# Kernel optimization log

Measured on AMD Instinct MI355X. Metric: run time of the kernel, lower is better.

## Reference

```python
import jax, jax.numpy as jnp
import numpy as np

T, B, M, H, NH = 4, 8, 1024, 768, 12
HD = H // NH
KMAX = 10


def _ln(x, s, b):
    mu = x.mean(-1, keepdims=True)
    var = ((x - mu) ** 2).mean(-1, keepdims=True)
    return (x - mu) * jax.lax.rsqrt(var + 1e-5) * s + b


def setup_inputs() -> dict:
    key = jax.random.key(0)
    ks = jax.random.split(key, 10)
    init = lambda k, shp: jax.random.normal(k, shp, jnp.float32) * 0.02
    return {
        'x': jax.random.normal(ks[0], (B, M, H), jnp.float32),
        'overlap': jax.random.randint(ks[1], (B, M, M), 0, KMAX + 1, jnp.int32),
        'lp': -jax.random.uniform(ks[2], (B, M), jnp.float32) * 10.0,
        'ln1_s': jnp.ones((T, H)), 'ln1_b': jnp.zeros((T, H)),
        'Wqkv': init(ks[3], (T, H, 3 * H)),
        'Wout': init(ks[4], (T, H, H)), 'bout': jnp.zeros((T, H)),
        'ln2_s': jnp.ones((T, H)), 'ln2_b': jnp.zeros((T, H)),
        'W1': init(ks[5], (T, H, 4 * H)), 'b1': jnp.zeros((T, 4 * H)),
        'W2': init(ks[6], (T, 4 * H, H)), 'b2': jnp.zeros((T, H)),
        'lno_s': jnp.ones((H,)), 'lno_b': jnp.zeros((H,)),
        'ov_emb': init(ks[7], (KMAX + 1,)),
        'ht_alpha': jnp.ones((1,), jnp.float32),
    }


def reference(x, overlap, lp, ln1_s, ln1_b, Wqkv, Wout, bout, ln2_s, ln2_b,
              W1, b1, W2, b2, lno_s, lno_b, ov_emb, ht_alpha):
    lp_c = jnp.clip(lp, -30.0, 0.0)                      # [B,M]
    ov = ov_emb[jnp.minimum(overlap, KMAX)]              # [B,M,M]
    bias = (ov - ht_alpha[0] * lp_c[:, None, :])[:, None]  # [B,1,M,M]
    scale = 1.0 / jnp.sqrt(jnp.float32(HD))
    for t in range(T):
        r = _ln(x, ln1_s[t], ln1_b[t])
        q, k, v = jnp.split(r @ Wqkv[t], 3, axis=-1)
        q = q.reshape(B, M, NH, HD).transpose(0, 2, 1, 3)
        k = k.reshape(B, M, NH, HD).transpose(0, 2, 1, 3)
        v = v.reshape(B, M, NH, HD).transpose(0, 2, 1, 3)
        s = jnp.einsum('bhqd,bhkd->bhqk', q, k) * scale + bias
        a = jax.nn.softmax(s, axis=-1)
        o = jnp.einsum('bhqk,bhkd->bhqd', a, v).transpose(0, 2, 1, 3).reshape(B, M, H)
        x = x + o @ Wout[t] + bout[t]
        h = _ln(x, ln2_s[t], ln2_b[t])
        x = x + jax.nn.gelu(h @ W1[t] + b1[t], approximate=False) @ W2[t] + b2[t]
    x = _ln(x, lno_s, lno_b)
    w = jax.nn.softmax(-lp_c, axis=1)                    # HT weights over m tokens
    return jnp.einsum('bm,bmh->bh', w, x)
```

## Files before the change

### kernel.cpp

```cpp
#include <hip/hip_runtime.h>
#include <hip/hip_bf16.h>
#include <math.h>

#define TT 4
#define BB 8
#define MM 1024
#define HH 768
#define NHEAD 12
#define HDIM 64
#define NTOK 8192
#define H3 2304
#define H4 3072

typedef __attribute__((ext_vector_type(8))) short bf16x8;
typedef __attribute__((ext_vector_type(4))) float f32x4;
typedef __attribute__((ext_vector_type(4))) unsigned short u16x4;

#define GLOBAL_AS(p) ((const __attribute__((address_space(1))) void*)(p))
#define LDS_AS(p)    ((__attribute__((address_space(3))) void*)(p))

__device__ __forceinline__ unsigned short f2bf(float f) {
  union { float f; unsigned u; } v; v.f = f;
  unsigned r = v.u + 0x7fffu + ((v.u >> 16) & 1u);
  return (unsigned short)(r >> 16);
}

__device__ __forceinline__ unsigned cvt_pk_bf16(float lo, float hi) {
  unsigned r;
  asm("v_cvt_pk_bf16_f32 %0, %1, %2" : "=v"(r) : "v"(lo), "v"(hi));
  return r;
}

__device__ __forceinline__ float fast_exp2(float x) {
#if __has_builtin(__builtin_amdgcn_exp2f)
  return __builtin_amdgcn_exp2f(x);
#else
  return exp2f(x);
#endif
}

__device__ __forceinline__ f32x4 mfma16(bf16x8 a, bf16x8 b, f32x4 c) {
  return __builtin_amdgcn_mfma_f32_16x16x32_bf16(a, b, c, 0, 0, 0);
}

__device__ __forceinline__ float block_sum256(float v, float* sh) {
  #pragma unroll
  for (int off = 32; off > 0; off >>= 1) v += __shfl_down(v, off);
  if ((threadIdx.x & 63) == 0) sh[threadIdx.x >> 6] = v;
  __syncthreads();
  v = sh[0] + sh[1] + sh[2] + sh[3];
  __syncthreads();
  return v;
}

__device__ __forceinline__ float block_max256(float v, float* sh) {
  #pragma unroll
  for (int off = 32; off > 0; off >>= 1) v = fmaxf(v, __shfl_down(v, off));
  if ((threadIdx.x & 63) == 0) sh[threadIdx.x >> 6] = v;
  __syncthreads();
  v = fmaxf(fmaxf(sh[0], sh[1]), fmaxf(sh[2], sh[3]));
  __syncthreads();
  return v;
}

__global__ __launch_bounds__(256) void wconv_kernel(const float* __restrict__ W,
                                                    unsigned short* __restrict__ Wt,
                                                    int K, int N) {
  __shared__ float tile[32][33];
  const int n0 = blockIdx.x * 32, k0 = blockIdx.y * 32;
  const int tx = threadIdx.x, ty = threadIdx.y;
  #pragma unroll
  for (int j = 0; j < 4; j++)
    tile[ty + j*8][tx] = W[(size_t)(k0 + ty + j*8) * N + n0 + tx];
  __syncthreads();
  #pragma unroll
  for (int j = 0; j < 4; j++)
    Wt[(size_t)(n0 + ty + j*8) * K + k0 + tx] = f2bf(tile[tx][ty + j*8]);
}

__global__ __launch_bounds__(256) void ln_kernel(const float* __restrict__ x,
                                                 const float* __restrict__ s,
                                                 const float* __restrict__ b,
                                                 unsigned short* __restrict__ out) {
  __shared__ float sh[4];
  const int row = blockIdx.x;
  const int tid = threadIdx.x;
  const float* xr = x + (size_t)row * HH;
  float v[3];
  float sum = 0.f;
  #pragma unroll
  for (int j = 0; j < 3; j++) { v[j] = xr[tid + j*256]; sum += v[j]; }
  sum = block_sum256(sum, sh);
  const float mu = sum * (1.f/768.f);
  float ss = 0.f;
  #pragma unroll
  for (int j = 0; j < 3; j++) { float d = v[j] - mu; ss += d*d; }
  ss = block_sum256(ss, sh);
  const float rstd = rsqrtf(ss * (1.f/768.f) + 1e-5f);
  #pragma unroll
  for (int j = 0; j < 3; j++) {
    int col = tid + j*256;
    out[(size_t)row * HH + col] = f2bf((v[j]-mu)*rstd*s[col] + b[col]);
  }
}

template<int EPI>
__global__ __launch_bounds__(256) void gemm_kernel(const unsigned short* __restrict__ A,
                                                   const unsigned short* __restrict__ Bt,
                                                   unsigned short* __restrict__ outB,
                                                   float* __restrict__ outF,
                                                   const float* __restrict__ bias,
                                                   int Ng, int Kg, int nx) {
  __shared__ unsigned short a_lds[2][128*64];
  __shared__ unsigned short b_lds[2][128*64];
  const int tid = threadIdx.x;
  const int w = tid >> 6, l = tid & 63;
  const int nwg = gridDim.x;
  const int lin = blockIdx.x;
  const int L = (lin & 7) * (nwg >> 3) + (lin >> 3);
  const int m0 = (L / nx) * 128, n0 = (L % nx) * 128;

  const int wr = (w >> 1) * 64, wc = (w & 1) * 64;
  const int l15 = l & 15, lhi = l >> 4;
  const int srow = w*32 + (l >> 3);
  const int schunk = (l & 7) ^ (l >> 3);
  const int scol = schunk << 3;

  f32x4 acc[4][4] = {};
  const int nk = Kg >> 6;
  int cur = 0;

  #pragma unroll
  for (int i = 0; i < 4; i++) {
    const unsigned short* gsa = A  + (size_t)(m0 + srow + i*8)*Kg + scol;
    const unsigned short* gsb = Bt + (size_t)(n0 + srow + i*8)*Kg + scol;
    __builtin_amdgcn_global_load_lds(GLOBAL_AS(gsa), LDS_AS(&a_lds[0][w*2048 + i*512]), 16, 0, 0);
    __builtin_amdgcn_global_load_lds(GLOBAL_AS(gsb), LDS_AS(&b_lds[0][w*2048 + i*512]), 16, 0, 0);
  }
  __syncthreads();

  for (int t = 0; t < nk; t++) {
    if (t + 1 < nk) {
      const int ks = (t + 1) << 6;
      #pragma unroll
      for (int i = 0; i < 4; i++) {
        const unsigned short* gsa = A  + (size_t)(m0 + srow + i*8)*Kg + ks + scol;
        const unsigned short* gsb = Bt + (size_t)(n0 + srow + i*8)*Kg + ks + scol;
        __builtin_amdgcn_global_load_lds(GLOBAL_AS(gsa), LDS_AS(&a_lds[cur^1][w*2048 + i*512]), 16, 0, 0);
        __builtin_amdgcn_global_load_lds(GLOBAL_AS(gsb), LDS_AS(&b_lds[cur^1][w*2048 + i*512]), 16, 0, 0);
      }
    }
    const unsigned short* ab = &a_lds[cur][0];
    const unsigned short* bb = &b_lds[cur][0];
    #pragma unroll
    for (int kb = 0; kb < 2; kb++) {
      bf16x8 af[4], bfr[4];
      const int rc = (kb*4 + lhi) ^ (l15 & 7);
      #pragma unroll
      for (int rb = 0; rb < 4; rb++)
        af[rb] = *(const bf16x8*)&ab[(wr + rb*16 + l15)*64 + (rc << 3)];
      #pragma unroll
      for (int nb = 0; nb < 4; nb++)
        bfr[nb] = *(const bf16x8*)&bb[(wc + nb*16 + l15)*64 + (rc << 3)];
      #pragma unroll
      for (int rb = 0; rb < 4; rb++)
        #pragma unroll
        for (int nb = 0; nb < 4; nb++)
          acc[rb][nb] = mfma16(af[rb], bfr[nb], acc[rb][nb]);
    }
    __syncthreads();
    cur ^= 1;
  }

  const int lr = lhi << 2;
  #pragma unroll
  for (int rb = 0; rb < 4; rb++)
    #pragma unroll
    for (int nb = 0; nb < 4; nb++) {
      const int row = m0 + wr + rb*16 + lr;
      const int col = n0 + wc + nb*16 + l15;
      #pragma unroll
      for (int r = 0; r < 4; r++) {
        float v = acc[rb][nb][r];
        const size_t off = (size_t)(row + r)*Ng + col;
        if (EPI == 0) {
          outB[off] = f2bf(v);
        } else if (EPI == 1) {
          v += bias[col];
          float u = 0.79788456080287f * v * (1.f + 0.044715f * v * v);
          u = fminf(u, 15.f);
          float e = fast_exp2(u * 2.88539008177793f);
          float th = 1.f - 2.f / (e + 1.f);
          v = 0.5f * v * (1.f + th);
          outB[off] = f2bf(v);
        } else {
          v += bias[col] + outF[off];
          outF[off] = v;
        }
      }
    }
}

__global__ __launch_bounds__(256) void biasprep_kernel(const int* __restrict__ overlap,
                                                       const float* __restrict__ lp,
                                                       const float* __restrict__ ov_emb,
                                                       const float* __restrict__ ht_alpha,
                                                       float* __restrict__ biasP) {
  __shared__ float oe[11];
  if (threadIdx.x < 11) oe[threadIdx.x] = ov_emb[threadIdx.x] * 1.44269504088896f;
  __syncthreads();
  const float aL = ht_alpha[0] * 1.44269504088896f;
  const size_t base = ((size_t)blockIdx.x * 256 + threadIdx.x) * 4;
  const int b = (int)(base >> 20);
  const int k0 = (int)(base & 1023);
  int4 ov = *(const int4*)&overlap[base];
  float4 lv = *(const float4*)&lp[b * MM + k0];
  float4 o4;
  {
    int t0 = ov.x < 10 ? ov.x : 10; float c0 = fminf(fmaxf(lv.x, -30.f), 0.f); o4.x = oe[t0] - aL*c0;
    int t1 = ov.y < 10 ? ov.y : 10; float c1 = fminf(fmaxf(lv.y, -30.f), 0.f); o4.y = oe[t1] - aL*c1;
    int t2 = ov.z < 10 ? ov.z : 10; float c2 = fminf(fmaxf(lv.z, -30.f), 0.f); o4.z = oe[t2] - aL*c2;
    int t3 = ov.w < 10 ? ov.w : 10; float c3 = fminf(fmaxf(lv.w, -30.f), 0.f); o4.w = oe[t3] - aL*c3;
  }
  *(float4*)&biasP[base] = o4;
}

__global__ __launch_bounds__(256) void attn_kernel(const unsigned short* __restrict__ qkv,
                                                   const float* __restrict__ biasP,
                                                   unsigned short* __restrict__ obuf) {
  __shared__ unsigned short k_lds[2][64*64];
  __shared__ unsigned short v_lds[2][64*64];
  __shared__ unsigned short pmat[4][32*64];

  const int tid = threadIdx.x;
  const int w = tid >> 6, l = tid & 63;
  const int lin = blockIdx.x;
  const int L = (lin & 7) * 96 + (lin >> 3);
  const int h = L % 12;
  const int qb = (L / 12) & 7;
  const int b = L / 96;
  const int q0w = qb*128 + w*32;
  const int l15 = l & 15, lhi = l >> 4;
  const float SC = 0.125f * 1.44269504088896f;

  const int kr_s = l >> 3;
  const int schunk = (l & 7) ^ kr_s;
  const int dc = (l & 7) << 3;

  bf16x8 qf[2][2];
  #pragma unroll
  for (int rb = 0; rb < 2; rb++)
    #pragma unroll
    for (int kb = 0; kb < 2; kb++)
      qf[rb][kb] = *(const bf16x8*)&qkv[(size_t)(b*MM + q0w + rb*16 + l15)*H3 + h*HDIM + kb*32 + lhi*8];

  const float* brow[2];
  #pragma unroll
  for (int rb = 0; rb < 2; rb++)
    brow[rb] = biasP + (size_t)(b*MM + q0w + rb*16 + l15) * MM;

  f32x4 oacc[4][2] = {};
  float mrow[2] = {-INFINITY, -INFINITY};
  float lrow[2] = {0.f, 0.f};

  bf16x8 vcur[2];
  {
    #pragma unroll
    for (int i = 0; i < 2; i++) {
      const unsigned short* g = qkv + (size_t)(b*MM + i*32 + w*8 + kr_s)*H3 + h*HDIM + HH + schunk*8;
      __builtin_amdgcn_global_load_lds(GLOBAL_AS(g), LDS_AS(&k_lds[0][(i*32 + w*8)*64]), 16, 0, 0);
    }
    bf16x8 vr[2];
    #pragma unroll
    for (int i = 0; i < 2; i++)
      vr[i] = *(const bf16x8*)&qkv[(size_t)(b*MM + i*32 + w*8 + kr_s)*H3 + h*HDIM + 2*HH + dc];
    #pragma unroll
    for (int i = 0; i < 2; i++) {
      int kr = i*32 + w*8 + kr_s;
      #pragma unroll
      for (int j = 0; j < 8; j++) {
        int key = ((((dc >> 3) & 7) ^ j) & 7) << 3;
        v_lds[0][(dc + j)*64 + (kr ^ key)] = (unsigned short)(short)vr[i][j];
      }
    }
    #pragma unroll
    for (int i = 0; i < 2; i++)
      vcur[i] = *(const bf16x8*)&qkv[(size_t)(b*MM + 64 + i*32 + w*8 + kr_s)*H3 + h*HDIM + 2*HH + dc];
    __syncthreads();
  }

  for (int kt = 0; kt < 16; kt++) {
    const int cur = kt & 1;
    const int kbase = kt * 64;

    if (kt < 15) {
      #pragma unroll
      for (int i = 0; i < 2; i++) {
        int kr = i*32 + w*8 + kr_s;
        #pragma unroll
        for (int j = 0; j < 8; j++) {
          int key = ((((dc >> 3) & 7) ^ j) & 7) << 3;
          v_lds[cur^1][(dc + j)*64 + (kr ^ key)] = (unsigned short)(short)vcur[i][j];
        }
      }
      const int nbase = kbase + 64;
      #pragma unroll
      for (int i = 0; i < 2; i++) {
        const unsigned short* g = qkv + (size_t)(b*MM + nbase + i*32 + w*8 + kr_s)*H3 + h*HDIM + HH + schunk*8;
        __builtin_amdgcn_global_load_lds(GLOBAL_AS(g), LDS_AS(&k_lds[cur^1][(i*32 + w*8)*64]), 16, 0, 0);
      }
    }
    if (kt < 14) {
      const int n2 = kbase + 128;
      #pragma unroll
      for (int i = 0; i < 2; i++)
        vcur[i] = *(const bf16x8*)&qkv[(size_t)(b*MM + n2 + i*32 + w*8 + kr_s)*H3 + h*HDIM + 2*HH + dc];
    }
    f32x4 bregs[4][2];
    #pragma unroll
    for (int nb = 0; nb < 4; nb++)
      #pragma unroll
      for (int rb = 0; rb < 2; rb++)
        bregs[nb][rb] = *(const f32x4*)&brow[rb][kbase + nb*16 + lhi*4];

    f32x4 sacc[4][2] = {};
    const unsigned short* kb_lds = &k_lds[cur][0];
    __builtin_amdgcn_s_setprio(1);
    #pragma unroll
    for (int kb = 0; kb < 2; kb++) {
      bf16x8 ak[4];
      #pragma unroll
      for (int nb = 0; nb < 4; nb++) {
        int n = nb*16 + l15;
        ak[nb] = *(const bf16x8*)&kb_lds[n*64 + ((kb*32 + lhi*8) ^ ((n & 7) << 3))];
      }
      #pragma unroll
      for (int nb = 0; nb < 4; nb++)
        #pragma unroll
        for (int rb = 0; rb < 2; rb++)
          sacc[nb][rb] = mfma16(ak[nb], qf[rb][kb], sacc[nb][rb]);
    }
    __builtin_amdgcn_s_setprio(0);

    #pragma unroll
    for (int nb = 0; nb < 4; nb++)
      #pragma unroll
      for (int rb = 0; rb < 2; rb++)
        #pragma unroll
        for (int r = 0; r < 4; r++)
          sacc[nb][rb][r] = fmaf(sacc[nb][rb][r], SC, bregs[nb][rb][r]);

    float corrf[2];
    int defer[2];
    #pragma unroll
    for (int rb = 0; rb < 2; rb++) {
      float pm = sacc[0][rb][0];
      #pragma unroll
      for (int nb = 0; nb < 4; nb++)
        #pragma unroll
        for (int r = 0; r < 4; r++)
          pm = fmaxf(pm, sacc[nb][rb][r]);
      pm = fmaxf(pm, __shfl_xor(pm, 16));
      pm = fmaxf(pm, __shfl_xor(pm, 32));
      defer[rb] = __all(pm - mrow[rb] <= 8.0f);
      const float mnew = defer[rb] ? mrow[rb] : fmaxf(mrow[rb], pm);
      const float corr = defer[rb] ? 1.0f : fast_exp2(mrow[rb] - mnew);
      float rs = 0.f;
      #pragma unroll
      for (int nb = 0; nb < 4; nb++)
        #pragma unroll
        for (int r = 0; r < 4; r++) {
          float p = fast_exp2(sacc[nb][rb][r] - mnew);
          sacc[nb][rb][r] = p;
          rs += p;
        }
      rs += __shfl_xor(rs, 16);
      rs += __shfl_xor(rs, 32);
      mrow[rb] = mnew;
      lrow[rb] = lrow[rb]*corr + rs;
      corrf[rb] = corr;
    }
    #pragma unroll
    for (int rb = 0; rb < 2; rb++)
      if (!defer[rb]) {
        #pragma unroll
        for (int db = 0; db < 4; db++)
          #pragma unroll
          for (int r = 0; r < 4; r++)
            oacc[db][rb][r] *= corrf[rb];
      }

    unsigned short* pw = &pmat[w][0];
    #pragma unroll
    for (int nb = 0; nb < 4; nb++)
      #pragma unroll
      for (int rb = 0; rb < 2; rb++) {
        uint2 pk;
        pk.x = cvt_pk_bf16(sacc[nb][rb][0], sacc[nb][rb][1]);
        pk.y = cvt_pk_bf16(sacc[nb][rb][2], sacc[nb][rb][3]);
        *(uint2*)&pw[(rb*16 + l15)*64 + ((nb*16 + lhi*4) ^ ((l15 & 7) << 3))] = pk;
      }

    const unsigned short* vb_lds = &v_lds[cur][0];
    __builtin_amdgcn_s_setprio(1);
    #pragma unroll
    for (int kb = 0; kb < 2; kb++) {
      bf16x8 pb[2];
      #pragma unroll
      for (int rb = 0; rb < 2; rb++)
        pb[rb] = *(const bf16x8*)&pw[(rb*16 + l15)*64 + ((kb*32 + lhi*8) ^ ((l15 & 7) << 3))];
      bf16x8 av[4];
      #pragma unroll
      for (int db = 0; db < 4; db++) {
        int d = db*16 + l15;
        int key = ((((d >> 3) & 7) ^ (d & 7)) & 7) << 3;
        av[db] = *(const bf16x8*)&vb_lds[d*64 + ((kb*32 + lhi*8) ^ key)];
      }
      #pragma unroll
      for (int db = 0; db < 4; db++)
        #pragma unroll
        for (int rb = 0; rb < 2; rb++)
          oacc[db][rb] = mfma16(av[db], pb[rb], oacc[db][rb]);
    }
    __builtin_amdgcn_s_setprio(0);

    __syncthreads();
  }

  float inv[2] = { 1.f / lrow[0], 1.f / lrow[1] };
  unsigned short* pw = &pmat[w][0];
  #pragma unroll
  for (int db = 0; db < 4; db++)
    #pragma unroll
    for (int rb = 0; rb < 2; rb++) {
      uint2 pk;
      pk.x = cvt_pk_bf16(oacc[db][rb][0] * inv[rb], oacc[db][rb][1] * inv[rb]);
      pk.y = cvt_pk_bf16(oacc[db][rb][2] * inv[rb], oacc[db][rb][3] * inv[rb]);
      *(uint2*)&pw[(rb*16 + l15)*64 + ((db*16 + lhi*4) ^ ((l15 & 7) << 3))] = pk;
    }
  #pragma unroll
  for (int rep = 0; rep < 4; rep++) {
    int qq = rep*8 + (l >> 3);
    int d0 = (l & 7) << 3;
    bf16x8 vv = *(const bf16x8*)&pw[qq*64 + (d0 ^ ((qq & 7) << 3))];
    *(bf16x8*)&obuf[(size_t)(b*MM + q0w + qq)*HH + h*HDIM + d0] = vv;
  }
}

__global__ __launch_bounds__(256) void htw_kernel(const float* __restrict__ lp,
                                                  float* __restrict__ w_ht) {
  __shared__ float sh[4];
  const int b = blockIdx.x, tid = threadIdx.x;
  float vals[4];
  float mx = -INFINITY;
  #pragma unroll
  for (int j = 0; j < 4; j++) {
    float lv = lp[b*MM + tid + j*256];
    float lc = fminf(fmaxf(lv, -30.f), 0.f);
    vals[j] = -lc;
    mx = fmaxf(mx, vals[j]);
  }
  mx = block_max256(mx, sh);
  float se = 0.f;
  #pragma unroll
  for (int j = 0; j < 4; j++) { vals[j] = expf(vals[j] - mx); se += vals[j]; }
  se = block_sum256(se, sh);
  const float inv = 1.f / se;
  #pragma unroll
  for (int j = 0; j < 4; j++) w_ht[b*MM + tid + j*256] = vals[j] * inv;
}

__global__ __launch_bounds__(256) void final_partial_kernel(const float* __restrict__ xbuf,
                                                            const float* __restrict__ lno_s,
                                                            const float* __restrict__ lno_b,
                                                            const float* __restrict__ w_ht,
                                                            float* __restrict__ part) {
  __shared__ float sh[4];
  const int b = blockIdx.x >> 4;
  const int chunk = blockIdx.x & 15;
  const int tid = threadIdx.x;
  float acc[3] = {0.f, 0.f, 0.f};
  float sc[3], bc[3];
  #pragma unroll
  for (int j = 0; j < 3; j++) { sc[j] = lno_s[tid + j*256]; bc[j] = lno_b[tid + j*256]; }
  for (int rr = 0; rr < 64; rr++) {
    const int tok = b*MM + chunk*64 + rr;
    const float* xr = xbuf + (size_t)tok * HH;
    float v[3]; float sum = 0.f;
    #pragma unroll
    for (int j = 0; j < 3; j++) { v[j] = xr[tid + j*256]; sum += v[j]; }
    sum = block_sum256(sum, sh);
    const float mu = sum * (1.f/768.f);
    float ss = 0.f;
    #pragma unroll
    for (int j = 0; j < 3; j++) { float d = v[j] - mu; ss += d*d; }
    ss = block_sum256(ss, sh);
    const float rstd = rsqrtf(ss * (1.f/768.f) + 1e-5f);
    const float wgt = w_ht[b*MM + chunk*64 + rr];
    #pragma unroll
    for (int j = 0; j < 3; j++) acc[j] += wgt * ((v[j]-mu)*rstd*sc[j] + bc[j]);
  }
  #pragma unroll
  for (int j = 0; j < 3; j++) part[(size_t)blockIdx.x * HH + tid + j*256] = acc[j];
}

__global__ __launch_bounds__(256) void final_reduce_kernel(const float* __restrict__ part,
                                                           float* __restrict__ out) {
  const int b = blockIdx.x;
  const int col = blockIdx.y*256 + threadIdx.x;
  float s = 0.f;
  #pragma unroll
  for (int c = 0; c < 16; c++) s += part[(size_t)(b*16 + c) * HH + col];
  out[b*HH + col] = s;
}

extern "C" void kernel_launch(void* const* d_in, const int* in_sizes, int n_in,
                              void* d_out, int out_size, void* d_ws, size_t ws_size,
                              hipStream_t stream) {
  (void)in_sizes; (void)n_in;
  const float* x      = (const float*)d_in[0];
  const int*   overlap= (const int*)d_in[1];
  const float* lp     = (const float*)d_in[2];
  const float* ln1_s  = (const float*)d_in[3];
  const float* ln1_b  = (const float*)d_in[4];
  const float* Wqkv   = (const float*)d_in[5];
  const float* Wout   = (const float*)d_in[6];
  const float* bout   = (const float*)d_in[7];
  const float* ln2_s  = (const float*)d_in[8];
  const float* ln2_b  = (const float*)d_in[9];
  const float* W1     = (const float*)d_in[10];
  const float* b1     = (const float*)d_in[11];
  const float* W2     = (const float*)d_in[12];
  const float* b2     = (const float*)d_in[13];
  const float* lno_s  = (const float*)d_in[14];
  const float* lno_b  = (const float*)d_in[15];
  const float* ov_emb = (const float*)d_in[16];
  const float* ht_alpha = (const float*)d_in[17];
  float* out = (float*)d_out;

  char* ws = (char*)d_ws;
  float*          xbuf  = (float*)(ws + 0);
  unsigned short* lnout = (unsigned short*)(ws + 25165824);
  unsigned short* qkv   = (unsigned short*)(ws + 37748736);
  unsigned short* obuf  = (unsigned short*)(ws + 75497472);
  unsigned short* gbuf  = (unsigned short*)(ws + 88080384);
  unsigned short* wbuf  = (unsigned short*)(ws + 138412032);
  float*          w_ht  = (float*)(ws + 143130624);
  float*          part  = (float*)(ws + 143163392);
  const int prep_once = (ws_size >= (size_t)143556608 + (size_t)33554432);
  float*          biasP = prep_once ? (float*)(ws + 143556608) : (float*)gbuf;

  hipMemcpyAsync(xbuf, x, (size_t)NTOK * HH * sizeof(float), hipMemcpyDeviceToDevice, stream);
  htw_kernel<<<BB, 256, 0, stream>>>(lp, w_ht);
  if (prep_once)
    biasprep_kernel<<<(BB*MM*MM/4)/256, 256, 0, stream>>>(overlap, lp, ov_emb, ht_alpha, biasP);

  for (int t = 0; t < TT; t++) {
    wconv_kernel<<<dim3(H3/32, HH/32), dim3(32, 8), 0, stream>>>(Wqkv + (size_t)t*HH*H3, wbuf, HH, H3);
    ln_kernel<<<NTOK, 256, 0, stream>>>(xbuf, ln1_s + t*HH, ln1_b + t*HH, lnout);
    gemm_kernel<0><<<(H3/128)*(NTOK/128), 256, 0, stream>>>(lnout, wbuf, qkv, nullptr, nullptr, H3, HH, H3/128);
    if (!prep_once)
      biasprep_kernel<<<(BB*MM*MM/4)/256, 256, 0, stream>>>(overlap, lp, ov_emb, ht_alpha, biasP);
    attn_kernel<<<BB*NHEAD*(MM/128), 256, 0, stream>>>(qkv, biasP, obuf);
    wconv_kernel<<<dim3(HH/32, HH/32), dim3(32, 8), 0, stream>>>(Wout + (size_t)t*HH*HH, wbuf, HH, HH);
    gemm_kernel<2><<<(HH/128)*(NTOK/128), 256, 0, stream>>>(obuf, wbuf, nullptr, xbuf, bout + t*HH, HH, HH, HH/128);
    ln_kernel<<<NTOK, 256, 0, stream>>>(xbuf, ln2_s + t*HH, ln2_b + t*HH, lnout);
    wconv_kernel<<<dim3(H4/32, HH/32), dim3(32, 8), 0, stream>>>(W1 + (size_t)t*HH*H4, wbuf, HH, H4);
    gemm_kernel<1><<<(H4/128)*(NTOK/128), 256, 0, stream>>>(lnout, wbuf, gbuf, nullptr, b1 + t*H4, H4, HH, H4/128);
    wconv_kernel<<<dim3(HH/32, H4/32), dim3(32, 8), 0, stream>>>(W2 + (size_t)t*H4*HH, wbuf, H4, HH);
    gemm_kernel<2><<<(HH/128)*(NTOK/128), 256, 0, stream>>>(gbuf, wbuf, nullptr, xbuf, b2 + t*HH, HH, H4, HH/128);
  }

  final_partial_kernel<<<BB*16, 256, 0, stream>>>(xbuf, lno_s, lno_b, w_ht, part);
  final_reduce_kernel<<<dim3(BB, 3), 256, 0, stream>>>(part, out);

  (void)out_size;
}
```

Baseline: 1.397 ms.

## Add 256x256 tiled 8-wave GEMM with pipelined LDS staging for QKV and FFN1

Adds a new GEMM kernel that computes 256x256 output tiles with 512 threads. It loads tiles straight from global memory into LDS with global_load_lds, using double buffering and interleaved vmcnt waits, and raises wave priority around the MFMA bursts. The kernel also remaps block indices in an XCD-aware order. The QKV projection and the FFN up-projection with GELU now use this kernel to get more data reuse per tile and better overlap of loads with MFMA. The cost is one block per CU, fewer blocks overall (288 and 384), and heavy register and LDS use.

```diff
diff --git a/kernel.cpp b/kernel.cpp
--- a/kernel.cpp
+++ b/kernel.cpp
@@ -196,6 +196,123 @@
         } else {
           v += bias[col] + outF[off];
           outF[off] = v;
+        }
+      }
+    }
+}
+
+#define PH_TAIL(MH, BFR) do {                                            \
+  __builtin_amdgcn_s_barrier();                                          \
+  asm volatile("s_waitcnt lgkmcnt(0)" ::: "memory");                     \
+  __builtin_amdgcn_sched_barrier(0);                                     \
+  __builtin_amdgcn_s_setprio(1);                                         \
+  _Pragma("unroll")                                                      \
+  for (int nf = 0; nf < 4; ++nf) {                                       \
+    _Pragma("unroll")                                                    \
+    for (int mf = 0; mf < 4; ++mf)                                       \
+      acc[(MH)*4+mf][nf] = mfma16(af[mf], BFR[nf], acc[(MH)*4+mf][nf]);  \
+  }                                                                      \
+  __builtin_amdgcn_s_setprio(0);                                         \
+  __builtin_amdgcn_s_barrier();                                          \
+} while (0)
+
+template<int EPI>
+__global__ __launch_bounds__(512, 1) void gemm256_kernel(const unsigned short* __restrict__ A,
+                                                         const unsigned short* __restrict__ Bt,
+                                                         unsigned short* __restrict__ outB,
+                                                         const float* __restrict__ bias,
+                                                         int Ng, int Kg, int nx) {
+  __shared__ unsigned short a_lds[2][2][256*32];
+  __shared__ unsigned short b_lds[2][2][256*32];
+  const int tid = threadIdx.x;
+  const int w = tid >> 6, l = tid & 63;
+  const int nwg = gridDim.x;
+  const int lin = blockIdx.x;
+  const int L = (lin & 7) * (nwg >> 3) + (lin >> 3);
+  const int m0 = (L / nx) * 256, n0 = (L % nx) * 256;
+  const int wm = w >> 2, wn = w & 3;
+  const int l15 = l & 15, lhi = l >> 4;
+
+  const int srow = tid >> 2;
+  const int scol = (tid & 3) << 3;
+
+  f32x4 acc[8][4] = {};
+  const int nk = Kg >> 6;
+
+  auto stageA = [&](int tt, int cb, int kk) {
+    #pragma unroll
+    for (int i = 0; i < 2; ++i) {
+      const unsigned short* g = A + (size_t)(m0 + i*128 + srow)*Kg + tt*64 + kk*32 + scol;
+      __builtin_amdgcn_global_load_lds(GLOBAL_AS(g), LDS_AS(&a_lds[cb][kk][i*4096 + tid*8]), 16, 0, 0);
+    }
+  };
+  auto stageB = [&](int tt, int cb, int kk) {
+    #pragma unroll
+    for (int i = 0; i < 2; ++i) {
+      const unsigned short* g = Bt + (size_t)(n0 + i*128 + srow)*Kg + tt*64 + kk*32 + scol;
+      __builtin_amdgcn_global_load_lds(GLOBAL_AS(g), LDS_AS(&b_lds[cb][kk][i*4096 + tid*8]), 16, 0, 0);
+    }
+  };
+  auto readA = [&](bf16x8* af, int cb, int kk, int mh) {
+    #pragma unroll
+    for (int mf = 0; mf < 4; ++mf)
+      af[mf] = *(const bf16x8*)&a_lds[cb][kk][(wm*128 + mh*64 + mf*16 + l15)*32 + lhi*8];
+  };
+  auto readB = [&](bf16x8* bf, int cb, int kk) {
+    #pragma unroll
+    for (int nf = 0; nf < 4; ++nf)
+      bf[nf] = *(const bf16x8*)&b_lds[cb][kk][(wn*64 + nf*16 + l15)*32 + lhi*8];
+  };
+
+  stageA(0, 0, 0); stageB(0, 0, 0);
+  stageA(0, 0, 1); stageB(0, 0, 1);
+  stageA(1, 1, 0); stageB(1, 1, 0);
+  asm volatile("s_waitcnt vmcnt(8)" ::: "memory");
+  __builtin_amdgcn_s_barrier();
+
+  for (int t = 0; t < nk; ++t) {
+    const int c = t & 1;
+    const int t1 = (t + 1 < nk) ? t + 1 : nk - 1;
+    const int t2 = (t + 2 < nk) ? t + 2 : nk - 1;
+    bf16x8 af[4], bfr0[4], bfr1[4];
+    readB(bfr0, c, 0);
+    readA(af, c, 0, 0);
+    stageA(t1, c ^ 1, 1);
+    PH_TAIL(0, bfr0);
+    readA(af, c, 0, 1);
+    stageB(t1, c ^ 1, 1);
+    asm volatile("s_waitcnt vmcnt(8)" ::: "memory");
+    PH_TAIL(1, bfr0);
+    readB(bfr1, c, 1);
+    readA(af, c, 1, 0);
+    stageA(t2, c, 0);
+    PH_TAIL(0, bfr1);
+    readA(af, c, 1, 1);
+    stageB(t2, c, 0);
+    asm volatile("s_waitcnt vmcnt(8)" ::: "memory");
+    PH_TAIL(1, bfr1);
+  }
+
+  #pragma unroll
+  for (int mfi = 0; mfi < 8; ++mfi)
+    #pragma unroll
+    for (int nf = 0; nf < 4; ++nf) {
+      const int row = m0 + wm*128 + (mfi >> 2)*64 + (mfi & 3)*16 + lhi*4;
+      const int col = n0 + wn*64 + nf*16 + l15;
+      #pragma unroll
+      for (int r = 0; r < 4; ++r) {
+        float v = acc[mfi][nf][r];
+        const size_t off = (size_t)(row + r)*Ng + col;
+        if (EPI == 0) {
+          outB[off] = f2bf(v);
+        } else {
+          v += bias[col];
+          float u = 0.79788456080287f * v * (1.f + 0.044715f * v * v);
+          u = fminf(u, 15.f);
+          float e = fast_exp2(u * 2.88539008177793f);
+          float th = 1.f - 2.f / (e + 1.f);
+          v = 0.5f * v * (1.f + th);
+          outB[off] = f2bf(v);
         }
       }
     }
@@ -558,7 +675,7 @@
   for (int t = 0; t < TT; t++) {
     wconv_kernel<<<dim3(H3/32, HH/32), dim3(32, 8), 0, stream>>>(Wqkv + (size_t)t*HH*H3, wbuf, HH, H3);
     ln_kernel<<<NTOK, 256, 0, stream>>>(xbuf, ln1_s + t*HH, ln1_b + t*HH, lnout);
-    gemm_kernel<0><<<(H3/128)*(NTOK/128), 256, 0, stream>>>(lnout, wbuf, qkv, nullptr, nullptr, H3, HH, H3/128);
+    gemm256_kernel<0><<<(H3/256)*(NTOK/256), 512, 0, stream>>>(lnout, wbuf, qkv, nullptr, H3, HH, H3/256);
     if (!prep_once)
       biasprep_kernel<<<(BB*MM*MM/4)/256, 256, 0, stream>>>(overlap, lp, ov_emb, ht_alpha, biasP);
     attn_kernel<<<BB*NHEAD*(MM/128), 256, 0, stream>>>(qkv, biasP, obuf);
@@ -566,7 +683,7 @@
     gemm_kernel<2><<<(HH/128)*(NTOK/128), 256, 0, stream>>>(obuf, wbuf, nullptr, xbuf, bout + t*HH, HH, HH, HH/128);
     ln_kernel<<<NTOK, 256, 0, stream>>>(xbuf, ln2_s + t*HH, ln2_b + t*HH, lnout);
     wconv_kernel<<<dim3(H4/32, HH/32), dim3(32, 8), 0, stream>>>(W1 + (size_t)t*HH*H4, wbuf, HH, H4);
-    gemm_kernel<1><<<(H4/128)*(NTOK/128), 256, 0, stream>>>(lnout, wbuf, gbuf, nullptr, b1 + t*H4, H4, HH, H4/128);
+    gemm256_kernel<1><<<(H4/256)*(NTOK/256), 512, 0, stream>>>(lnout, wbuf, gbuf, b1 + t*H4, H4, HH, H4/256);
     wconv_kernel<<<dim3(HH/32, H4/32), dim3(32, 8), 0, stream>>>(W2 + (size_t)t*H4*HH, wbuf, H4, HH);
     gemm_kernel<2><<<(HH/128)*(NTOK/128), 256, 0, stream>>>(gbuf, wbuf, nullptr, xbuf, b2 + t*HH, HH, H4, HH/128);
   }
```

Measured after the change: 1.501 ms. 7.5% more time.

## Add 256x128 triple-buffered GEMM for QKV and FFN1 projections

Applied to the files above, without the earlier changes.

Adds a new GEMM kernel with 512 threads, a 256x128 output tile per workgroup, and a three-stage LDS ring filled by direct global-to-LDS loads with swizzled layout. It is used for the QKV and W1 (GELU) projections in place of the 128x128 kernel. The larger tile raises operand reuse, and the deeper prefetch overlaps memory loads with MFMA work. In exchange, LDS use (~144KB) and register pressure limit occupancy to one workgroup per CU, and the grid-index remap changes tile ordering.

```diff
diff --git a/kernel.cpp b/kernel.cpp
--- a/kernel.cpp
+++ b/kernel.cpp
@@ -196,6 +196,104 @@
         } else {
           v += bias[col] + outF[off];
           outF[off] = v;
+        }
+      }
+    }
+}
+
+template<int EPI>
+__global__ __launch_bounds__(512, 1) void gemm256x128_kernel(const unsigned short* __restrict__ A,
+                                                             const unsigned short* __restrict__ Bt,
+                                                             unsigned short* __restrict__ outB,
+                                                             const float* __restrict__ bias,
+                                                             int Ng, int Kg, int nx) {
+  __shared__ unsigned short a_lds[3][256*64];
+  __shared__ unsigned short b_lds[3][128*64];
+  const int tid = threadIdx.x;
+  const int w = tid >> 6, l = tid & 63;
+  const int nwg = gridDim.x;
+  const int lin = blockIdx.x;
+  const int L = (lin & 7) * (nwg >> 3) + (lin >> 3);
+  const int m0 = (L / nx) * 256, n0 = (L % nx) * 128;
+  const int wm = w >> 1, wn = w & 1;
+  const int l15 = l & 15, lhi = l >> 4;
+
+  const int srow = tid >> 3;
+  const int scol = ((tid & 7) ^ (srow & 7)) << 3;
+
+  f32x4 acc[4][4] = {};
+  const int nk = Kg >> 6;
+
+  auto stage = [&](int tt, int cb) {
+    const int ks = tt << 6;
+    #pragma unroll
+    for (int i = 0; i < 4; ++i) {
+      const unsigned short* g = A + (size_t)(m0 + i*64 + srow)*Kg + ks + scol;
+      __builtin_amdgcn_global_load_lds(GLOBAL_AS(g), LDS_AS(&a_lds[cb][i*4096 + tid*8]), 16, 0, 0);
+    }
+    #pragma unroll
+    for (int i = 0; i < 2; ++i) {
+      const unsigned short* g = Bt + (size_t)(n0 + i*64 + srow)*Kg + ks + scol;
+      __builtin_amdgcn_global_load_lds(GLOBAL_AS(g), LDS_AS(&b_lds[cb][i*4096 + tid*8]), 16, 0, 0);
+    }
+  };
+
+  stage(0, 0);
+  stage(1, 1);
+  asm volatile("s_waitcnt vmcnt(6)" ::: "memory");
+  __builtin_amdgcn_s_barrier();
+  __builtin_amdgcn_sched_barrier(0);
+
+  for (int t = 0; t < nk; ++t) {
+    if (t + 2 < nk) stage(t + 2, (t + 2) % 3);
+    __builtin_amdgcn_sched_barrier(0);
+
+    const unsigned short* ab = &a_lds[t % 3][0];
+    const unsigned short* bb = &b_lds[t % 3][0];
+    #pragma unroll
+    for (int kb = 0; kb < 2; ++kb) {
+      bf16x8 af[4], bfr[4];
+      const int rc8 = ((kb*4 + lhi) ^ (l15 & 7)) << 3;
+      #pragma unroll
+      for (int mf = 0; mf < 4; ++mf)
+        af[mf] = *(const bf16x8*)&ab[(wm*64 + mf*16 + l15)*64 + rc8];
+      #pragma unroll
+      for (int nf = 0; nf < 4; ++nf)
+        bfr[nf] = *(const bf16x8*)&bb[(wn*64 + nf*16 + l15)*64 + rc8];
+      #pragma unroll
+      for (int mf = 0; mf < 4; ++mf)
+        #pragma unroll
+        for (int nf = 0; nf < 4; ++nf)
+          acc[mf][nf] = mfma16(af[mf], bfr[nf], acc[mf][nf]);
+    }
+
+    __builtin_amdgcn_sched_barrier(0);
+    if (t + 2 < nk) { asm volatile("s_waitcnt vmcnt(6)" ::: "memory"); }
+    else            { asm volatile("s_waitcnt vmcnt(0)" ::: "memory"); }
+    __builtin_amdgcn_s_barrier();
+    __builtin_amdgcn_sched_barrier(0);
+  }
+
+  #pragma unroll
+  for (int mf = 0; mf < 4; ++mf)
+    #pragma unroll
+    for (int nf = 0; nf < 4; ++nf) {
+      const int row = m0 + wm*64 + mf*16 + lhi*4;
+      const int col = n0 + wn*64 + nf*16 + l15;
+      #pragma unroll
+      for (int r = 0; r < 4; ++r) {
+        float v = acc[mf][nf][r];
+        const size_t off = (size_t)(row + r)*Ng + col;
+        if (EPI == 0) {
+          outB[off] = f2bf(v);
+        } else {
+          v += bias[col];
+          float u = 0.79788456080287f * v * (1.f + 0.044715f * v * v);
+          u = fminf(u, 15.f);
+          float e = fast_exp2(u * 2.88539008177793f);
+          float th = 1.f - 2.f / (e + 1.f);
+          v = 0.5f * v * (1.f + th);
+          outB[off] = f2bf(v);
         }
       }
     }
@@ -558,7 +656,7 @@
   for (int t = 0; t < TT; t++) {
     wconv_kernel<<<dim3(H3/32, HH/32), dim3(32, 8), 0, stream>>>(Wqkv + (size_t)t*HH*H3, wbuf, HH, H3);
     ln_kernel<<<NTOK, 256, 0, stream>>>(xbuf, ln1_s + t*HH, ln1_b + t*HH, lnout);
-    gemm_kernel<0><<<(H3/128)*(NTOK/128), 256, 0, stream>>>(lnout, wbuf, qkv, nullptr, nullptr, H3, HH, H3/128);
+    gemm256x128_kernel<0><<<(NTOK/256)*(H3/128), 512, 0, stream>>>(lnout, wbuf, qkv, nullptr, H3, HH, H3/128);
     if (!prep_once)
       biasprep_kernel<<<(BB*MM*MM/4)/256, 256, 0, stream>>>(overlap, lp, ov_emb, ht_alpha, biasP);
     attn_kernel<<<BB*NHEAD*(MM/128), 256, 0, stream>>>(qkv, biasP, obuf);
@@ -566,7 +664,7 @@
     gemm_kernel<2><<<(HH/128)*(NTOK/128), 256, 0, stream>>>(obuf, wbuf, nullptr, xbuf, bout + t*HH, HH, HH, HH/128);
     ln_kernel<<<NTOK, 256, 0, stream>>>(xbuf, ln2_s + t*HH, ln2_b + t*HH, lnout);
     wconv_kernel<<<dim3(H4/32, HH/32), dim3(32, 8), 0, stream>>>(W1 + (size_t)t*HH*H4, wbuf, HH, H4);
-    gemm_kernel<1><<<(H4/128)*(NTOK/128), 256, 0, stream>>>(lnout, wbuf, gbuf, nullptr, b1 + t*H4, H4, HH, H4/128);
+    gemm256x128_kernel<1><<<(NTOK/256)*(H4/128), 512, 0, stream>>>(lnout, wbuf, gbuf, b1 + t*H4, H4, HH, H4/128);
     wconv_kernel<<<dim3(HH/32, H4/32), dim3(32, 8), 0, stream>>>(W2 + (size_t)t*H4*HH, wbuf, H4, HH);
     gemm_kernel<2><<<(HH/128)*(NTOK/128), 256, 0, stream>>>(gbuf, wbuf, nullptr, xbuf, b2 + t*HH, HH, H4, HH/128);
   }
```

Result: slower. 1.484 ms (+6.2%).

## Split attention over key halves and merge partials in a second kernel

Applied to the files above, without the earlier changes.

Attention is split across two key halves (split-K / flash-decoding style), doubling the grid from 768 to 1536 blocks so more CUs stay busy. Each half writes unnormalized fp32 partial outputs plus row max/sum, and a new merge kernel rescales and combines them into bf16 obuf. The price is extra global traffic for the fp32 partials (about 50MB per layer) and one more kernel launch, and the gbuf and wbuf scratch buffers are reused to hold the partials. The new path runs only when the workspace is large enough for the precomputed bias.

```diff
diff --git a/kernel.cpp b/kernel.cpp
--- a/kernel.cpp
+++ b/kernel.cpp
@@ -225,9 +225,12 @@
   *(float4*)&biasP[base] = o4;
 }
 
+template<int SPLIT>
 __global__ __launch_bounds__(256) void attn_kernel(const unsigned short* __restrict__ qkv,
                                                    const float* __restrict__ biasP,
-                                                   unsigned short* __restrict__ obuf) {
+                                                   unsigned short* __restrict__ obuf,
+                                                   float* __restrict__ opart,
+                                                   float* __restrict__ ml) {
   __shared__ unsigned short k_lds[2][64*64];
   __shared__ unsigned short v_lds[2][64*64];
   __shared__ unsigned short pmat[4][32*64];
@@ -235,10 +238,24 @@
   const int tid = threadIdx.x;
   const int w = tid >> 6, l = tid & 63;
   const int lin = blockIdx.x;
-  const int L = (lin & 7) * 96 + (lin >> 3);
-  const int h = L % 12;
-  const int qb = (L / 12) & 7;
-  const int b = L / 96;
+  int h, qb, b, half;
+  if (SPLIT) {
+    const int L = (lin & 7) * 192 + (lin >> 3);
+    h = L % 12;
+    const int rest = L / 12;
+    qb = rest & 7;
+    const int bp = rest >> 3;
+    b = bp & 7;
+    half = bp >> 3;
+  } else {
+    const int L = (lin & 7) * 96 + (lin >> 3);
+    h = L % 12;
+    qb = (L / 12) & 7;
+    b = L / 96;
+    half = 0;
+  }
+  const int nkt = SPLIT ? 8 : 16;
+  const int kt0 = half * 8;
   const int q0w = qb*128 + w*32;
   const int l15 = l & 15, lhi = l >> 4;
   const float SC = 0.125f * 1.44269504088896f;
@@ -265,15 +282,16 @@
 
   bf16x8 vcur[2];
   {
+    const int kb0 = kt0 * 64;
     #pragma unroll
     for (int i = 0; i < 2; i++) {
-      const unsigned short* g = qkv + (size_t)(b*MM + i*32 + w*8 + kr_s)*H3 + h*HDIM + HH + schunk*8;
+      const unsigned short* g = qkv + (size_t)(b*MM + kb0 + i*32 + w*8 + kr_s)*H3 + h*HDIM + HH + schunk*8;
       __builtin_amdgcn_global_load_lds(GLOBAL_AS(g), LDS_AS(&k_lds[0][(i*32 + w*8)*64]), 16, 0, 0);
     }
     bf16x8 vr[2];
     #pragma unroll
     for (int i = 0; i < 2; i++)
-      vr[i] = *(const bf16x8*)&qkv[(size_t)(b*MM + i*32 + w*8 + kr_s)*H3 + h*HDIM + 2*HH + dc];
+      vr[i] = *(const bf16x8*)&qkv[(size_t)(b*MM + kb0 + i*32 + w*8 + kr_s)*H3 + h*HDIM + 2*HH + dc];
     #pragma unroll
     for (int i = 0; i < 2; i++) {
       int kr = i*32 + w*8 + kr_s;
@@ -285,22 +303,22 @@
     }
     #pragma unroll
     for (int i = 0; i < 2; i++)
-      vcur[i] = *(const bf16x8*)&qkv[(size_t)(b*MM + 64 + i*32 + w*8 + kr_s)*H3 + h*HDIM + 2*HH + dc];
+      vcur[i] = *(const bf16x8*)&qkv[(size_t)(b*MM + kb0 + 64 + i*32 + w*8 + kr_s)*H3 + h*HDIM + 2*HH + dc];
     __syncthreads();
   }
 
-  for (int kt = 0; kt < 16; kt++) {
-    const int cur = kt & 1;
-    const int kbase = kt * 64;
-
-    if (kt < 15) {
+  for (int j = 0; j < nkt; j++) {
+    const int cur = j & 1;
+    const int kbase = (kt0 + j) * 64;
+
+    if (j < nkt - 1) {
       #pragma unroll
       for (int i = 0; i < 2; i++) {
         int kr = i*32 + w*8 + kr_s;
         #pragma unroll
-        for (int j = 0; j < 8; j++) {
-          int key = ((((dc >> 3) & 7) ^ j) & 7) << 3;
-          v_lds[cur^1][(dc + j)*64 + (kr ^ key)] = (unsigned short)(short)vcur[i][j];
+        for (int jj = 0; jj < 8; jj++) {
+          int key = ((((dc >> 3) & 7) ^ jj) & 7) << 3;
+          v_lds[cur^1][(dc + jj)*64 + (kr ^ key)] = (unsigned short)(short)vcur[i][jj];
         }
       }
       const int nbase = kbase + 64;
@@ -310,7 +328,7 @@
         __builtin_amdgcn_global_load_lds(GLOBAL_AS(g), LDS_AS(&k_lds[cur^1][(i*32 + w*8)*64]), 16, 0, 0);
       }
     }
-    if (kt < 14) {
+    if (j < nkt - 2) {
       const int n2 = kbase + 128;
       #pragma unroll
       for (int i = 0; i < 2; i++)
@@ -427,23 +445,71 @@
     __syncthreads();
   }
 
-  float inv[2] = { 1.f / lrow[0], 1.f / lrow[1] };
-  unsigned short* pw = &pmat[w][0];
-  #pragma unroll
-  for (int db = 0; db < 4; db++)
-    #pragma unroll
-    for (int rb = 0; rb < 2; rb++) {
-      uint2 pk;
-      pk.x = cvt_pk_bf16(oacc[db][rb][0] * inv[rb], oacc[db][rb][1] * inv[rb]);
-      pk.y = cvt_pk_bf16(oacc[db][rb][2] * inv[rb], oacc[db][rb][3] * inv[rb]);
-      *(uint2*)&pw[(rb*16 + l15)*64 + ((db*16 + lhi*4) ^ ((l15 & 7) << 3))] = pk;
-    }
-  #pragma unroll
-  for (int rep = 0; rep < 4; rep++) {
-    int qq = rep*8 + (l >> 3);
-    int d0 = (l & 7) << 3;
-    bf16x8 vv = *(const bf16x8*)&pw[qq*64 + (d0 ^ ((qq & 7) << 3))];
-    *(bf16x8*)&obuf[(size_t)(b*MM + q0w + qq)*HH + h*HDIM + d0] = vv;
+  if (SPLIT) {
+    const int bh = b*12 + h;
+    const int hb = half*96 + bh;
+    if (l < 16) {
+      #pragma unroll
+      for (int rb = 0; rb < 2; rb++) {
+        const int q = q0w + rb*16 + l15;
+        float2 v2; v2.x = mrow[rb]; v2.y = lrow[rb];
+        ((float2*)ml)[(size_t)hb*1024 + q] = v2;
+      }
+    }
+    #pragma unroll
+    for (int db = 0; db < 4; db++)
+      #pragma unroll
+      for (int rb = 0; rb < 2; rb++) {
+        const int q = q0w + rb*16 + l15;
+        const int d0 = db*16 + lhi*4;
+        *(f32x4*)&opart[((size_t)hb*1024 + q)*64 + d0] = oacc[db][rb];
+      }
+  } else {
+    float inv[2] = { 1.f / lrow[0], 1.f / lrow[1] };
+    unsigned short* pw = &pmat[w][0];
+    #pragma unroll
+    for (int db = 0; db < 4; db++)
+      #pragma unroll
+      for (int rb = 0; rb < 2; rb++) {
+        uint2 pk;
+        pk.x = cvt_pk_bf16(oacc[db][rb][0] * inv[rb], oacc[db][rb][1] * inv[rb]);
+        pk.y = cvt_pk_bf16(oacc[db][rb][2] * inv[rb], oacc[db][rb][3] * inv[rb]);
+        *(uint2*)&pw[(rb*16 + l15)*64 + ((db*16 + lhi*4) ^ ((l15 & 7) << 3))] = pk;
+      }
+    #pragma unroll
+    for (int rep = 0; rep < 4; rep++) {
+      int qq = rep*8 + (l >> 3);
+      int d0 = (l & 7) << 3;
+      bf16x8 vv = *(const bf16x8*)&pw[qq*64 + (d0 ^ ((qq & 7) << 3))];
+      *(bf16x8*)&obuf[(size_t)(b*MM + q0w + qq)*HH + h*HDIM + d0] = vv;
+    }
+  }
+}
+
+__global__ __launch_bounds__(256) void attn_merge_kernel(const float* __restrict__ opart,
+                                                         const float* __restrict__ ml,
+                                                         unsigned short* __restrict__ obuf) {
+  const int tid = threadIdx.x;
+  const int w = tid >> 6, l = tid & 63;
+  const int bh = blockIdx.x >> 4, qg = blockIdx.x & 15;
+  const int b = bh / 12, h = bh % 12;
+  const int d0 = (l & 15) * 4;
+  #pragma unroll
+  for (int r = 0; r < 4; r++) {
+    const int q = qg*64 + r*16 + w*4 + (l >> 4);
+    float2 ml0 = ((const float2*)ml)[(size_t)(0*96 + bh)*1024 + q];
+    float2 ml1 = ((const float2*)ml)[(size_t)(1*96 + bh)*1024 + q];
+    const float ms = fmaxf(ml0.x, ml1.x);
+    float s0 = fast_exp2(ml0.x - ms);
+    float s1 = fast_exp2(ml1.x - ms);
+    const float inv = 1.f / (ml0.y*s0 + ml1.y*s1);
+    s0 *= inv; s1 *= inv;
+    f32x4 o0 = *(const f32x4*)&opart[((size_t)(0*96 + bh)*1024 + q)*64 + d0];
+    f32x4 o1 = *(const f32x4*)&opart[((size_t)(1*96 + bh)*1024 + q)*64 + d0];
+    uint2 pk;
+    pk.x = cvt_pk_bf16(o0[0]*s0 + o1[0]*s1, o0[1]*s0 + o1[1]*s1);
+    pk.y = cvt_pk_bf16(o0[2]*s0 + o1[2]*s1, o0[3]*s0 + o1[3]*s1);
+    *(uint2*)&obuf[(size_t)(b*MM + q)*HH + h*HDIM + d0] = pk;
   }
 }
 
@@ -549,6 +615,8 @@
   float*          part  = (float*)(ws + 143163392);
   const int prep_once = (ws_size >= (size_t)143556608 + (size_t)33554432);
   float*          biasP = prep_once ? (float*)(ws + 143556608) : (float*)gbuf;
+  float*          opart = (float*)gbuf;
+  float*          mlbuf = (float*)wbuf;
 
   hipMemcpyAsync(xbuf, x, (size_t)NTOK * HH * sizeof(float), hipMemcpyDeviceToDevice, stream);
   htw_kernel<<<BB, 256, 0, stream>>>(lp, w_ht);
@@ -559,9 +627,13 @@
     wconv_kernel<<<dim3(H3/32, HH/32), dim3(32, 8), 0, stream>>>(Wqkv + (size_t)t*HH*H3, wbuf, HH, H3);
     ln_kernel<<<NTOK, 256, 0, stream>>>(xbuf, ln1_s + t*HH, ln1_b + t*HH, lnout);
     gemm_kernel<0><<<(H3/128)*(NTOK/128), 256, 0, stream>>>(lnout, wbuf, qkv, nullptr, nullptr, H3, HH, H3/128);
-    if (!prep_once)
+    if (prep_once) {
+      attn_kernel<1><<<2*BB*NHEAD*(MM/128), 256, 0, stream>>>(qkv, biasP, nullptr, opart, mlbuf);
+      attn_merge_kernel<<<BB*NHEAD*(MM/64), 256, 0, stream>>>(opart, mlbuf, obuf);
+    } else {
       biasprep_kernel<<<(BB*MM*MM/4)/256, 256, 0, stream>>>(overlap, lp, ov_emb, ht_alpha, biasP);
-    attn_kernel<<<BB*NHEAD*(MM/128), 256, 0, stream>>>(qkv, biasP, obuf);
+      attn_kernel<0><<<BB*NHEAD*(MM/128), 256, 0, stream>>>(qkv, biasP, obuf, nullptr, nullptr);
+    }
     wconv_kernel<<<dim3(HH/32, HH/32), dim3(32, 8), 0, stream>>>(Wout + (size_t)t*HH*HH, wbuf, HH, HH);
     gemm_kernel<2><<<(HH/128)*(NTOK/128), 256, 0, stream>>>(obuf, wbuf, nullptr, xbuf, bout + t*HH, HH, HH, HH/128);
     ln_kernel<<<NTOK, 256, 0, stream>>>(xbuf, ln2_s + t*HH, ln2_b + t*HH, lnout);
```

After: 1.416 ms. Within noise of the previous version (+1.4%).
